# Kernel optimization log

Measured on AMD Instinct MI355X. Metric: run time of the kernel, lower is better.

Reference implementation:

```python
import jax, jax.numpy as jnp
import numpy as np

B, N, C, H = 32, 384, 768, 12
EPS = 1e-6

def setup_inputs() -> dict:
    key = jax.random.key(0)
    k0, k1, k2, k3 = jax.random.split(key, 4)
    x = jax.random.normal(k0, (B, N, C), dtype=jnp.float32)
    # binary keep-mask over key tokens, broadcastable to [B,1,N,N]
    policy = (jax.random.uniform(k1, (B, 1, 1, N)) > 0.5).astype(jnp.float32)
    qkv_w = jax.random.normal(k2, (3 * C, C), dtype=jnp.float32) * 0.02
    qkv_b = jnp.zeros((3 * C,), dtype=jnp.float32)
    proj_w = jax.random.normal(k3, (C, C), dtype=jnp.float32) * 0.02
    proj_b = jnp.zeros((C,), dtype=jnp.float32)
    return {"x": x, "policy": policy, "qkv_w": qkv_w, "qkv_b": qkv_b,
            "proj_w": proj_w, "proj_b": proj_b}

def reference(x, policy, qkv_w, qkv_b, proj_w, proj_b):
    b, n, c = x.shape
    hd = c // H
    scale = hd ** -0.5
    qkv = (x @ qkv_w.T + qkv_b).reshape(b, n, 3, H, hd).transpose(2, 0, 3, 1, 4)
    q, k, v = qkv[0], qkv[1], qkv[2]
    attn = jnp.einsum('bhnd,bhmd->bhnm', q, k) * scale  # [B,H,N,N]
    # softmax_with_policy: eye-blend so every token attends to itself,
    # then eps-regularized masked softmax
    eye = jnp.eye(n, dtype=policy.dtype)[None, None]  # [1,1,N,N]
    attn_policy = policy + (1.0 - policy) * eye       # broadcast -> [B,1,N,N]
    max_att = attn.max(axis=-1, keepdims=True)
    e = jnp.exp(attn - max_att) * attn_policy
    attn = (e + EPS / n) / (e.sum(axis=-1, keepdims=True) + EPS)
    out = jnp.einsum('bhnm,bhmd->bnhd', attn, v).reshape(b, n, c)
    return out @ proj_w.T + proj_b
```

## Files before the change

kernel.cpp:

```cpp
#include <hip/hip_runtime.h>

#define BB 32
#define NN 384
#define CC 768
#define HH 12
#define HD 64

typedef __attribute__((ext_vector_type(4))) float f32x4;
typedef __attribute__((ext_vector_type(8))) __bf16 bf16x8;
typedef __attribute__((ext_vector_type(4))) __bf16 bf16x4;

static __device__ __forceinline__ f32x4 mfma16(bf16x8 a, bf16x8 b, f32x4 c) {
    return __builtin_amdgcn_mfma_f32_16x16x32_bf16(a, b, c, 0, 0, 0);
}

static __device__ __forceinline__ void gload_lds16(const void* g, void* l) {
    __builtin_amdgcn_global_load_lds((const __attribute__((address_space(1))) void*)g,
                                     (__attribute__((address_space(3))) void*)l, 16, 0, 0);
}

#define XU   1179648
#define QU   73728
#define QKVU 221184
#define PU   73728
__global__ void cvt_kernel(const float* __restrict__ x, const float* __restrict__ qkv_w,
                           const float* __restrict__ proj_w, __bf16* __restrict__ dst) {
    const int i = blockIdx.x * blockDim.x + threadIdx.x;
    if (i >= XU + QKVU + PU) return;
    const float* src;
    float sc = 1.f;
    if (i < XU) src = x + (size_t)i * 8;
    else if (i < XU + QKVU) {
        src = qkv_w + (size_t)(i - XU) * 8;
        if (i < XU + QU) sc = 0.125f;
    } else src = proj_w + (size_t)(i - XU - QKVU) * 8;
    f32x4 a = *(const f32x4*)src;
    f32x4 b = *(const f32x4*)(src + 4);
    bf16x8 o;
#pragma unroll
    for (int j = 0; j < 4; ++j) { o[j] = (__bf16)(a[j] * sc); o[j + 4] = (__bf16)(b[j] * sc); }
    *(bf16x8*)(dst + (size_t)i * 8) = o;
}

template <int EPI>
__global__ __launch_bounds__(256, 4) void gemm_kernel(
    const __bf16* __restrict__ A, const __bf16* __restrict__ Bw,
    const float* __restrict__ bias,
    __bf16* __restrict__ qkbuf, __bf16* __restrict__ vtbuf,
    float* __restrict__ fout) {
    __shared__ __bf16 Alds[128 * 64];
    __shared__ __bf16 Blds[128 * 64];

    const int tid = threadIdx.x;
    const int l = tid & 63;
    const int w = tid >> 6;
    const int g = l >> 4, q16 = l & 15;
    const int mb = blockIdx.x * 128;
    const int nb = blockIdx.y * 128;
    const int wrb = (w >> 1) * 64;
    const int wcb = (w & 1) * 64;
    const int srow = w * 8 + (l >> 3);
    const int scol = (l & 7) * 8;

    f32x4 acc[4][4] = {};

    for (int kt = 0; kt < 12; ++kt) {
        const int kof = kt * 64 + scol;
#pragma unroll
        for (int i = 0; i < 4; ++i) {
            gload_lds16(&A[(size_t)(mb + i * 32 + srow) * CC + kof], &Alds[i * 2048 + w * 512]);
            gload_lds16(&Bw[(size_t)(nb + i * 32 + srow) * CC + kof], &Blds[i * 2048 + w * 512]);
        }
        __syncthreads();
#pragma unroll
        for (int c = 0; c < 2; ++c) {
            bf16x8 af[4], bfr[4];
#pragma unroll
            for (int m = 0; m < 4; ++m)
                af[m] = *(const bf16x8*)&Alds[(wrb + m * 16 + q16) * 64 + c * 32 + g * 8];
#pragma unroll
            for (int n = 0; n < 4; ++n)
                bfr[n] = *(const bf16x8*)&Blds[(wcb + n * 16 + q16) * 64 + c * 32 + g * 8];
#pragma unroll
            for (int m = 0; m < 4; ++m)
#pragma unroll
                for (int n = 0; n < 4; ++n)
                    acc[m][n] = mfma16(af[m], bfr[n], acc[m][n]);
        }
        __syncthreads();
    }

    if constexpr (EPI == 0) {
        const int bbatch = mb / NN;
        const int tokb = mb % NN;
#pragma unroll
        for (int n = 0; n < 4; ++n) {
            const int colb = nb + wcb + n * 16;
            const int col = colb + q16;
            float bs = bias[col];
            if (colb < 2 * CC) {
                if (colb < CC) bs *= 0.125f;
#pragma unroll
                for (int m = 0; m < 4; ++m) {
                    const int row = mb + wrb + m * 16 + g * 4;
#pragma unroll
                    for (int r = 0; r < 4; ++r)
                        qkbuf[(size_t)(row + r) * 1536 + col] = (__bf16)(acc[m][n][r] + bs);
                }
            } else {
                const int dd = (col - 2 * CC) & 63;
                const int hh = (colb - 2 * CC) >> 6;
                __bf16* vp = vtbuf + ((size_t)(bbatch * HH + hh) * HD + dd) * NN;
#pragma unroll
                for (int m = 0; m < 4; ++m) {
                    const int tok = tokb + wrb + m * 16 + g * 4;
                    bf16x4 pk;
#pragma unroll
                    for (int r = 0; r < 4; ++r) pk[r] = (__bf16)(acc[m][n][r] + bs);
                    *(bf16x4*)&vp[tok] = pk;
                }
            }
        }
    } else {
#pragma unroll
        for (int n = 0; n < 4; ++n) {
            const int col = nb + wcb + n * 16 + q16;
            const float bs = bias[col];
#pragma unroll
            for (int m = 0; m < 4; ++m)
#pragma unroll
                for (int r = 0; r < 4; ++r)
                    fout[(size_t)(mb + wrb + m * 16 + g * 4 + r) * CC + col] = acc[m][n][r] + bs;
        }
    }
}

__global__ __launch_bounds__(512, 1) void attn_kernel(
    const __bf16* __restrict__ qkbuf, const __bf16* __restrict__ vtbuf,
    const float* __restrict__ policy, __bf16* __restrict__ attb) {
    __shared__ __bf16 Qlds[NN * HD];
    __shared__ __bf16 Klds[NN * HD];
    __shared__ __bf16 Vlds[HD * NN];
    __shared__ float pol[NN];

    const int tid = threadIdx.x;
    const int l = tid & 63;
    const int w = tid >> 6;
    const int g = l >> 4, q16 = l & 15;
    const int bh = blockIdx.x;
    const int b = bh / HH, h = bh % HH;

    const __bf16* qg = qkbuf + (size_t)b * NN * 1536 + h * HD;
    const __bf16* kg = qg + CC;
#pragma unroll
    for (int p = 0; p < 6; ++p) {
        const int cs = p * 512 + w * 64 + l;
        const int row = cs >> 3, cin = cs & 7;
        const size_t go = (size_t)row * 1536 + (size_t)((cin ^ (row & 7)) << 3);
        gload_lds16(&qg[go], &Qlds[(p * 512 + w * 64) * 8]);
        gload_lds16(&kg[go], &Klds[(p * 512 + w * 64) * 8]);
    }
    const __bf16* vg = vtbuf + (size_t)(b * HH + h) * HD * NN;
#pragma unroll
    for (int p = 0; p < 6; ++p) {
        const int cs = p * 512 + w * 64 + l;
        const int row = cs / 48, cin = cs - row * 48;
        gload_lds16(&vg[row * NN + ((cin ^ (row & 7)) << 3)], &Vlds[(p * 512 + w * 64) * 8]);
    }
    for (int i = tid; i < NN; i += 512) pol[i] = policy[b * NN + i];
    __syncthreads();

    const int sw = (q16 & 7) << 4;

#pragma unroll 1
    for (int ps = 0; ps < 3; ++ps) {
        const int qrow = ps * 128 + w * 16 + q16;
        const int qbyte0 = qrow * 128 + g * 16;
        const bf16x8 qf0 = *(const bf16x8*)((const char*)Qlds + (qbyte0 ^ sw));
        const bf16x8 qf1 = *(const bf16x8*)((const char*)Qlds + ((qbyte0 + 64) ^ sw));

        float m = -1e30f, sum = 0.f;
        f32x4 oacc[4] = {};

#pragma unroll 1
        for (int kt = 0; kt < 6; ++kt) {
            f32x4 st[4];
            __builtin_amdgcn_s_setprio(1);
#pragma unroll
            for (int t = 0; t < 4; ++t) {
                const int byte0 = ((kt * 4 + t) * 16 + q16) * 128 + g * 16;
                bf16x8 k0 = *(const bf16x8*)((const char*)Klds + (byte0 ^ sw));
                bf16x8 k1 = *(const bf16x8*)((const char*)Klds + ((byte0 + 64) ^ sw));
                f32x4 z = {0.f, 0.f, 0.f, 0.f};
                st[t] = mfma16(k1, qf1, mfma16(k0, qf0, z));
            }
            __builtin_amdgcn_s_setprio(0);

            float tmx = fmaxf(fmaxf(st[0][0], st[0][1]), fmaxf(st[0][2], st[0][3]));
#pragma unroll
            for (int t = 1; t < 4; ++t)
#pragma unroll
                for (int r = 0; r < 4; ++r) tmx = fmaxf(tmx, st[t][r]);
            tmx = fmaxf(tmx, __shfl_xor(tmx, 16));
            tmx = fmaxf(tmx, __shfl_xor(tmx, 32));

            const float newm = fmaxf(m, tmx);
            const float f = __expf(m - newm);
            m = newm;
            sum *= f;
#pragma unroll
            for (int db = 0; db < 4; ++db) oacc[db] *= f;

#pragma unroll
            for (int t = 0; t < 4; ++t)
#pragma unroll
                for (int r = 0; r < 4; ++r) {
                    const int key = kt * 64 + t * 16 + g * 4 + r;
                    const bool keep = (pol[key] > 0.5f) || (key == qrow);
                    const float e = keep ? __expf(st[t][r] - m) : 0.f;
                    st[t][r] = e;
                    sum += e;
                }

            __builtin_amdgcn_s_setprio(1);
#pragma unroll
            for (int c4 = 0; c4 < 2; ++c4) {
                bf16x8 pf;
#pragma unroll
                for (int r = 0; r < 4; ++r) {
                    pf[r] = (__bf16)st[2 * c4][r];
                    pf[r + 4] = (__bf16)st[2 * c4 + 1][r];
                }
                const int c = kt * 2 + c4;
#pragma unroll
                for (int db = 0; db < 4; ++db) {
                    const int byte0 = (db * 16 + q16) * 768 + c * 64 + g * 8;
                    bf16x4 v0 = *(const bf16x4*)((const char*)Vlds + (byte0 ^ sw));
                    bf16x4 v1 = *(const bf16x4*)((const char*)Vlds + ((byte0 + 32) ^ sw));
                    bf16x8 vf;
#pragma unroll
                    for (int r = 0; r < 4; ++r) { vf[r] = v0[r]; vf[r + 4] = v1[r]; }
                    oacc[db] = mfma16(vf, pf, oacc[db]);
                }
            }
            __builtin_amdgcn_s_setprio(0);
        }

        sum += __shfl_xor(sum, 16);
        sum += __shfl_xor(sum, 32);
        const float dinv = 1.f / (sum + 1e-6f);

        __bf16* op = attb + ((size_t)b * NN + qrow) * CC + h * HD;
#pragma unroll
        for (int db = 0; db < 4; ++db) {
            bf16x4 pk;
#pragma unroll
            for (int r = 0; r < 4; ++r) pk[r] = (__bf16)(oacc[db][r] * dinv);
            *(bf16x4*)&op[db * 16 + g * 4] = pk;
        }
    }
}

extern "C" void kernel_launch(void* const* d_in, const int* in_sizes, int n_in,
                              void* d_out, int out_size, void* d_ws, size_t ws_size,
                              hipStream_t stream) {
    (void)in_sizes; (void)n_in; (void)out_size; (void)ws_size;
    const float* x      = (const float*)d_in[0];
    const float* policy = (const float*)d_in[1];
    const float* qkv_w  = (const float*)d_in[2];
    const float* qkv_b  = (const float*)d_in[3];
    const float* proj_w = (const float*)d_in[4];
    const float* proj_b = (const float*)d_in[5];
    float* out = (float*)d_out;

    __bf16* xb    = (__bf16*)d_ws;
    __bf16* wqkv  = xb + (size_t)12288 * 768;
    __bf16* wproj = wqkv + (size_t)2304 * 768;
    __bf16* qkbuf = wproj + (size_t)768 * 768;
    __bf16* vtbuf = qkbuf + (size_t)12288 * 1536;
    __bf16* attb  = vtbuf + (size_t)BB * HH * HD * NN;

    const int units = XU + QKVU + PU;
    cvt_kernel<<<(units + 255) / 256, 256, 0, stream>>>(x, qkv_w, proj_w, xb);

    gemm_kernel<0><<<dim3(96, 18), 256, 0, stream>>>(xb, wqkv, qkv_b, qkbuf, vtbuf, nullptr);
    attn_kernel<<<384, 512, 0, stream>>>(qkbuf, vtbuf, policy, attb);
    gemm_kernel<1><<<dim3(96, 6), 256, 0, stream>>>(attb, wproj, proj_b, nullptr, nullptr, out);
}
```

Measured before the change: 150.3 us.

## Add triple-buffered swizzled 256x128 QKV GEMM with direct-to-LDS loads

Replaces the QKV projection GEMM with a dedicated kernel that uses 256x128 tiles and 512 threads. Global tiles are loaded straight into LDS through a three-buffer ring, so the next tiles arrive while the current one is multiplied. Reads use an XOR swizzle to avoid LDS bank conflicts, and wave priority is raised around the MFMA bursts. The larger LDS footprint leaves one block per CU, which lowers occupancy in exchange for more data reuse and overlap.

```diff
diff --git a/kernel.cpp b/kernel.cpp
--- a/kernel.cpp
+++ b/kernel.cpp
@@ -42,6 +42,122 @@
     *(bf16x8*)(dst + (size_t)i * 8) = o;
 }
 
+__global__ __launch_bounds__(512, 1) void gemm0_kernel(
+    const __bf16* __restrict__ A, const __bf16* __restrict__ Bw,
+    const float* __restrict__ bias,
+    __bf16* __restrict__ qkbuf, __bf16* __restrict__ vtbuf) {
+    __shared__ __bf16 SA[3][256 * 64];
+    __shared__ __bf16 SB[3][128 * 64];
+
+    const int tid = threadIdx.x;
+    const int l = tid & 63;
+    const int w = tid >> 6;
+    const int g = l >> 4, q16 = l & 15;
+    const int wm = w >> 1, wn = w & 1;
+    const int mb = blockIdx.x * 256;
+    const int nb = blockIdx.y * 128;
+    const int swz = q16 & 7;
+
+    auto stageA = [&](int buf, int kt) {
+#pragma unroll
+        for (int j = 0; j < 4; ++j) {
+            const int ci = j * 512 + w * 64 + l;
+            const int row = ci >> 3, c = ci & 7;
+            gload_lds16(&A[(size_t)(mb + row) * CC + kt * 64 + ((c ^ (row & 7)) << 3)],
+                        &SA[buf][(j * 512 + w * 64) * 8]);
+        }
+    };
+    auto stageB = [&](int buf, int kt) {
+#pragma unroll
+        for (int j = 0; j < 2; ++j) {
+            const int ci = j * 512 + w * 64 + l;
+            const int row = ci >> 3, c = ci & 7;
+            gload_lds16(&Bw[(size_t)(nb + row) * CC + kt * 64 + ((c ^ (row & 7)) << 3)],
+                        &SB[buf][(j * 512 + w * 64) * 8]);
+        }
+    };
+
+    f32x4 acc[4][4] = {};
+
+    stageA(0, 0); stageB(0, 0);
+    stageA(1, 1); stageB(1, 1);
+
+#pragma unroll 1
+    for (int t = 0; t < 12; ++t) {
+        const int ts = (t + 2 <= 11) ? t + 2 : 11;
+        stageA((t + 2) % 3, ts);
+        stageB((t + 2) % 3, ts);
+        asm volatile("s_waitcnt vmcnt(12)" ::: "memory");
+        asm volatile("s_barrier" ::: "memory");
+
+        const char* pa = (const char*)&SA[t % 3][0];
+        const char* pb = (const char*)&SB[t % 3][0];
+
+        bf16x8 af[4], bfr[4];
+#pragma unroll
+        for (int m = 0; m < 4; ++m)
+            af[m] = *(const bf16x8*)(pa + (wm * 64 + m * 16 + q16) * 128 + ((g ^ swz) << 4));
+#pragma unroll
+        for (int n = 0; n < 4; ++n)
+            bfr[n] = *(const bf16x8*)(pb + (wn * 64 + n * 16 + q16) * 128 + ((g ^ swz) << 4));
+        __builtin_amdgcn_s_setprio(1);
+#pragma unroll
+        for (int m = 0; m < 4; ++m)
+#pragma unroll
+            for (int n = 0; n < 4; ++n)
+                acc[m][n] = mfma16(af[m], bfr[n], acc[m][n]);
+        __builtin_amdgcn_s_setprio(0);
+
+#pragma unroll
+        for (int m = 0; m < 4; ++m)
+            af[m] = *(const bf16x8*)(pa + (wm * 64 + m * 16 + q16) * 128 + (((4 + g) ^ swz) << 4));
+#pragma unroll
+        for (int n = 0; n < 4; ++n)
+            bfr[n] = *(const bf16x8*)(pb + (wn * 64 + n * 16 + q16) * 128 + (((4 + g) ^ swz) << 4));
+        asm volatile("s_waitcnt lgkmcnt(0)" ::: "memory");
+        __builtin_amdgcn_sched_barrier(0);
+        asm volatile("s_barrier" ::: "memory");
+        __builtin_amdgcn_s_setprio(1);
+#pragma unroll
+        for (int m = 0; m < 4; ++m)
+#pragma unroll
+            for (int n = 0; n < 4; ++n)
+                acc[m][n] = mfma16(af[m], bfr[n], acc[m][n]);
+        __builtin_amdgcn_s_setprio(0);
+    }
+
+#pragma unroll
+    for (int n = 0; n < 4; ++n) {
+        const int colb = nb + wn * 64 + n * 16;
+        const int col = colb + q16;
+        float bs = bias[col];
+        if (colb < 2 * CC) {
+            if (colb < CC) bs *= 0.125f;
+#pragma unroll
+            for (int m = 0; m < 4; ++m) {
+                const int row = mb + wm * 64 + m * 16 + g * 4;
+#pragma unroll
+                for (int r = 0; r < 4; ++r)
+                    qkbuf[(size_t)(row + r) * 1536 + col] = (__bf16)(acc[m][n][r] + bs);
+            }
+        } else {
+            const int dd = (col - 2 * CC) & 63;
+            const int hh = (colb - 2 * CC) >> 6;
+#pragma unroll
+            for (int m = 0; m < 4; ++m) {
+                const int row = mb + wm * 64 + m * 16 + g * 4;
+                const int bbatch = row / NN;
+                const int tok = row - bbatch * NN;
+                __bf16* vp = vtbuf + ((size_t)(bbatch * HH + hh) * HD + dd) * NN;
+                bf16x4 pk;
+#pragma unroll
+                for (int r = 0; r < 4; ++r) pk[r] = (__bf16)(acc[m][n][r] + bs);
+                *(bf16x4*)&vp[tok] = pk;
+            }
+        }
+    }
+}
+
 template <int EPI>
 __global__ __launch_bounds__(256, 4) void gemm_kernel(
     const __bf16* __restrict__ A, const __bf16* __restrict__ Bw,
@@ -90,49 +206,17 @@
         __syncthreads();
     }
 
-    if constexpr (EPI == 0) {
-        const int bbatch = mb / NN;
-        const int tokb = mb % NN;
-#pragma unroll
-        for (int n = 0; n < 4; ++n) {
-            const int colb = nb + wcb + n * 16;
-            const int col = colb + q16;
-            float bs = bias[col];
-            if (colb < 2 * CC) {
-                if (colb < CC) bs *= 0.125f;
-#pragma unroll
-                for (int m = 0; m < 4; ++m) {
-                    const int row = mb + wrb + m * 16 + g * 4;
-#pragma unroll
-                    for (int r = 0; r < 4; ++r)
-                        qkbuf[(size_t)(row + r) * 1536 + col] = (__bf16)(acc[m][n][r] + bs);
-                }
-            } else {
-                const int dd = (col - 2 * CC) & 63;
-                const int hh = (colb - 2 * CC) >> 6;
-                __bf16* vp = vtbuf + ((size_t)(bbatch * HH + hh) * HD + dd) * NN;
-#pragma unroll
-                for (int m = 0; m < 4; ++m) {
-                    const int tok = tokb + wrb + m * 16 + g * 4;
-                    bf16x4 pk;
-#pragma unroll
-                    for (int r = 0; r < 4; ++r) pk[r] = (__bf16)(acc[m][n][r] + bs);
-                    *(bf16x4*)&vp[tok] = pk;
-                }
-            }
-        }
-    } else {
-#pragma unroll
-        for (int n = 0; n < 4; ++n) {
-            const int col = nb + wcb + n * 16 + q16;
-            const float bs = bias[col];
-#pragma unroll
-            for (int m = 0; m < 4; ++m)
-#pragma unroll
-                for (int r = 0; r < 4; ++r)
-                    fout[(size_t)(mb + wrb + m * 16 + g * 4 + r) * CC + col] = acc[m][n][r] + bs;
-        }
-    }
+#pragma unroll
+    for (int n = 0; n < 4; ++n) {
+        const int col = nb + wcb + n * 16 + q16;
+        const float bs = bias[col];
+#pragma unroll
+        for (int m = 0; m < 4; ++m)
+#pragma unroll
+            for (int r = 0; r < 4; ++r)
+                fout[(size_t)(mb + wrb + m * 16 + g * 4 + r) * CC + col] = acc[m][n][r] + bs;
+    }
+    (void)qkbuf; (void)vtbuf;
 }
 
 __global__ __launch_bounds__(512, 1) void attn_kernel(
@@ -283,7 +367,7 @@
     const int units = XU + QKVU + PU;
     cvt_kernel<<<(units + 255) / 256, 256, 0, stream>>>(x, qkv_w, proj_w, xb);
 
-    gemm_kernel<0><<<dim3(96, 18), 256, 0, stream>>>(xb, wqkv, qkv_b, qkbuf, vtbuf, nullptr);
+    gemm0_kernel<<<dim3(48, 18), 512, 0, stream>>>(xb, wqkv, qkv_b, qkbuf, vtbuf);
     attn_kernel<<<384, 512, 0, stream>>>(qkbuf, vtbuf, policy, attb);
     gemm_kernel<1><<<dim3(96, 6), 256, 0, stream>>>(attb, wproj, proj_b, nullptr, nullptr, out);
 }
```

Measured after the change: 168.8 us. 1.12x slower.
